# Optimization experiments

Hardware: AMD Instinct MI355X
Metric: run time of the kernel (lower is better)

Reference implementation:

```python
import jax, jax.numpy as jnp
import numpy as np
import math

B, T, D, H = 4, 2048, 1024, 8
DK = D // H


def _rel_shift(x):
    # x: [B, H, T, P] with P = 2T-1 (Transformer-XL relative shift)
    b, h, q, p = x.shape
    x = jnp.pad(x, ((0, 0), (0, 0), (0, 0), (1, 0)))
    x = x.reshape(b, h, p + 1, q)[:, :, 1:]
    return x.reshape(b, h, q, p)


def setup_inputs() -> dict:
    key = jax.random.key(0)
    ks = jax.random.split(key, 9)
    s = 0.02
    x = jax.random.normal(ks[0], (B, T, D), jnp.float32)
    pos_emb = jax.random.normal(ks[1], (1, 2 * T - 1, D), jnp.float32)
    Wq = jax.random.normal(ks[2], (D, D), jnp.float32) * s
    Wk = jax.random.normal(ks[3], (D, D), jnp.float32) * s
    Wv = jax.random.normal(ks[4], (D, D), jnp.float32) * s
    Wo = jax.random.normal(ks[5], (D, D), jnp.float32) * s
    Wp = jax.random.normal(ks[6], (D, D), jnp.float32) * s
    pos_bias_u = jax.random.normal(ks[7], (H, DK), jnp.float32) * s
    pos_bias_v = jax.random.normal(ks[8], (H, DK), jnp.float32) * s
    return {"x": x, "pos_emb": pos_emb, "Wq": Wq, "Wk": Wk, "Wv": Wv,
            "Wo": Wo, "Wp": Wp, "pos_bias_u": pos_bias_u, "pos_bias_v": pos_bias_v}


def reference(x, pos_emb, Wq, Wk, Wv, Wo, Wp, pos_bias_u, pos_bias_v):
    b, t, d = x.shape
    h, dk = pos_bias_u.shape
    inv_sdk = 1.0 / math.sqrt(dk)
    # projections (torch Linear: y = x @ W.T)
    q = (x @ Wq.T).reshape(b, t, h, dk)          # [B,T,H,DK]
    k = (x @ Wk.T).reshape(b, t, h, dk)          # [B,T,H,DK]
    v = (x @ Wv.T).reshape(b, t, h, dk)          # [B,T,H,DK]
    p = (pos_emb @ Wp.T).reshape(-1, h, dk)      # [P,H,DK], P = 2T-1
    # content and position scores
    matrix_ac = jnp.einsum('bqhd,bkhd->bhqk', q + pos_bias_u, k)   # [B,H,T,T]
    matrix_bd = jnp.einsum('bqhd,phd->bhqp', q + pos_bias_v, p)    # [B,H,T,2T-1]
    matrix_bd = _rel_shift(matrix_bd)[..., :t]                     # [B,H,T,T]
    scores = (matrix_ac + matrix_bd) * inv_sdk
    attn = jax.nn.softmax(scores, axis=-1)
    out = jnp.einsum('bhqk,bkhd->bqhd', attn, v).reshape(b, t, h * dk)
    return out @ Wo.T
```

## Files before the change

kernel.cpp:

```cpp
#include <hip/hip_runtime.h>
#include <cstdint>
#include <math.h>

#define B_   4
#define T_   2048
#define D_   1024
#define H_   8
#define DK_  128
#define P_   4095
#define PS_  4096

typedef unsigned short ushort_t;
typedef __attribute__((ext_vector_type(8))) short short8;
typedef __attribute__((ext_vector_type(4))) float floatx4;

__device__ inline float bf2f(ushort_t s) {
    return __uint_as_float(((unsigned int)s) << 16);
}
__device__ inline ushort_t f2bf(float f) {
    unsigned int u = __float_as_uint(f);
    u += 0x7fffu + ((u >> 16) & 1u);
    return (ushort_t)(u >> 16);
}

__device__ inline floatx4 mfma16(short8 a, short8 b, floatx4 c) {
    return __builtin_amdgcn_mfma_f32_16x16x32_bf16(a, b, c, 0, 0, 0);
}

__device__ inline void gload_lds16(const ushort_t* g, ushort_t* l) {
    __builtin_amdgcn_global_load_lds(
        (const __attribute__((address_space(1))) unsigned int*)g,
        (__attribute__((address_space(3))) unsigned int*)l, 16, 0, 0);
}

__global__ void detect_kernel(const ushort_t* x, int* flag) {
    if (blockIdx.x == 0 && threadIdx.x == 0) {
        int m = 0;
        for (int i = 0; i < 64; ++i) {
            float v = bf2f(x[2 * i]);
            float a = fabsf(v);
            if (!(a == 0.0f || (a > 1e-20f && a < 1e10f))) m = 1;
        }
        flag[0] = m;
    }
}

#define CV_TOT 17826816
template <int MODE>
__global__ __launch_bounds__(256) void convert_kernel(
    const int* __restrict__ flag,
    const void* __restrict__ x, const void* __restrict__ pe,
    const void* __restrict__ wq, const void* __restrict__ wk,
    const void* __restrict__ wv, const void* __restrict__ wo,
    const void* __restrict__ wp, const void* __restrict__ ub,
    const void* __restrict__ vb, ushort_t* __restrict__ dst)
{
    if (flag[0] != MODE) return;
    const size_t i = ((size_t)blockIdx.x * 256 + threadIdx.x) * 4;
    if (i >= CV_TOT) return;
    const void* s; size_t off;
    if (i < 8388608)       { s = x;  off = i; }
    else if (i < 12581888) { s = pe; off = i - 8388608; }
    else if (i < 13630464) { s = wq; off = i - 12581888; }
    else if (i < 14679040) { s = wk; off = i - 13630464; }
    else if (i < 15727616) { s = wv; off = i - 14679040; }
    else if (i < 16776192) { s = wo; off = i - 15727616; }
    else if (i < 17824768) { s = wp; off = i - 16776192; }
    else if (i < 17825792) { s = ub; off = i - 17824768; }
    else                   { s = vb; off = i - 17825792; }
    const size_t d = i + (i >= 12581888 ? 1024 : 0);
    if (MODE == 0) {
        *(uint2*)(dst + d) = *(const uint2*)((const ushort_t*)s + off);
    } else {
        float4 f = *(const float4*)((const float*)s + off);
        uint2 o;
        o.x = (unsigned)f2bf(f.x) | ((unsigned)f2bf(f.y) << 16);
        o.y = (unsigned)f2bf(f.z) | ((unsigned)f2bf(f.w) << 16);
        *(uint2*)(dst + d) = o;
    }
}

__global__ __launch_bounds__(256, 3) void gemm_mfma(
    const int* __restrict__ flag,
    const ushort_t* __restrict__ A, const ushort_t* __restrict__ W,
    void* __restrict__ C, int smode)
{
    if (smode == 3 && flag[0] != 0) return;
    if (smode == 4 && flag[0] != 1) return;
    const int K = 1024, N = 1024;

    __shared__ ushort_t Al[128 * 32];
    __shared__ ushort_t Wl[128 * 32];

    const int tid  = threadIdx.x;
    const int w    = tid >> 6, lane = tid & 63;
    const int r15  = lane & 15, quad = lane >> 4;
    const int wm   = w >> 1, wn = w & 1;
    const int m0   = blockIdx.y * 128, n0 = blockIdx.x * 128;

    floatx4 acc[4][4];
    const floatx4 z4 = {0.f, 0.f, 0.f, 0.f};
#pragma unroll
    for (int mt = 0; mt < 4; ++mt)
#pragma unroll
        for (int nt = 0; nt < 4; ++nt) acc[mt][nt] = z4;

    for (int k0 = 0; k0 < K; k0 += 32) {
#pragma unroll
        for (int it = 0; it < 2; ++it) {
            const int rbase = w * 32 + it * 16;
            const int row   = rbase + (lane >> 2);
            const int c     = (lane & 3) ^ ((row >> 1) & 3);
            gload_lds16(A + (size_t)(m0 + row) * K + k0 + c * 8, &Al[rbase * 32]);
            gload_lds16(W + (size_t)(n0 + row) * K + k0 + c * 8, &Wl[rbase * 32]);
        }
        __syncthreads();

        short8 af[4], bf[4];
#pragma unroll
        for (int mt = 0; mt < 4; ++mt) {
            const int row  = wm * 64 + mt * 16 + r15;
            const int slot = quad ^ ((row >> 1) & 3);
            af[mt] = *(const short8*)&Al[row * 32 + slot * 8];
        }
#pragma unroll
        for (int nt = 0; nt < 4; ++nt) {
            const int row  = wn * 64 + nt * 16 + r15;
            const int slot = quad ^ ((row >> 1) & 3);
            bf[nt] = *(const short8*)&Wl[row * 32 + slot * 8];
        }
#pragma unroll
        for (int mt = 0; mt < 4; ++mt)
#pragma unroll
            for (int nt = 0; nt < 4; ++nt)
                acc[mt][nt] = mfma16(af[mt], bf[nt], acc[mt][nt]);
        __syncthreads();
    }

#pragma unroll
    for (int mt = 0; mt < 4; ++mt)
#pragma unroll
        for (int nt = 0; nt < 4; ++nt)
#pragma unroll
            for (int i = 0; i < 4; ++i) {
                const int m = m0 + wm * 64 + mt * 16 + quad * 4 + i;
                const int n = n0 + wn * 64 + nt * 16 + r15;
                const float v = acc[mt][nt][i];
                if (smode == 0) {
                    const int b = m >> 11, t = m & (T_ - 1);
                    const int h = n >> 7, dk = n & (DK_ - 1);
                    ((ushort_t*)C)[(((size_t)(b * H_ + h)) * T_ + t) * DK_ + dk] = f2bf(v);
                } else if (smode == 1) {
                    const int h = n >> 7, dk = n & (DK_ - 1);
                    ((ushort_t*)C)[((size_t)h * PS_ + m) * DK_ + dk] = f2bf(v);
                } else if (smode == 2) {
                    const int b = m >> 11, t = m & (T_ - 1);
                    const int h = n >> 7, dk = n & (DK_ - 1);
                    ((ushort_t*)C)[((size_t)(b * H_ + h) * DK_ + dk) * T_ + t] = f2bf(v);
                } else if (smode == 3) {
                    ((ushort_t*)C)[(size_t)m * N + n] = f2bf(v);
                } else {
                    ((float*)C)[(size_t)m * N + n] = v;
                }
            }
}

__global__ __launch_bounds__(256, 2) void attn_mfma(
    const ushort_t* __restrict__ qg,
    const ushort_t* __restrict__ kgl,
    const ushort_t* __restrict__ vt,
    const ushort_t* __restrict__ pg,
    const ushort_t* __restrict__ ubb,
    const ushort_t* __restrict__ vbb,
    ushort_t* __restrict__ ao)
{
    __shared__ ushort_t K_lds[64 * 128];
    __shared__ ushort_t V_lds[128 * 64];
    __shared__ float bd_lds[4][16][84];
    __shared__ __align__(16) ushort_t pr_lds[4][16][72];

    const int tid  = threadIdx.x;
    const int w    = tid >> 6;
    const int lane = tid & 63;
    const int r15  = lane & 15;
    const int quad = lane >> 4;
    const int bh   = blockIdx.y;
    const int h    = bh & (H_ - 1);
    const int b    = bh >> 3;
    const int q0w  = blockIdx.x * 64 + w * 16;

    short8 quA[4], qvA[4];
    {
        const ushort_t* qrow = qg + ((size_t)bh * T_ + q0w + r15) * DK_;
#pragma unroll
        for (int ks = 0; ks < 4; ++ks) {
            const int dk0 = ks * 32 + quad * 8;
            uint4 q4 = *(const uint4*)(qrow + dk0);
            uint4 u4 = *(const uint4*)(ubb + (size_t)h * DK_ + dk0);
            uint4 v4 = *(const uint4*)(vbb + (size_t)h * DK_ + dk0);
            const ushort_t* qs = (const ushort_t*)&q4;
            const ushort_t* us = (const ushort_t*)&u4;
            const ushort_t* vs = (const ushort_t*)&v4;
#pragma unroll
            for (int j = 0; j < 8; ++j) {
                const float qf = bf2f(qs[j]);
                quA[ks][j] = (short)f2bf(qf + bf2f(us[j]));
                qvA[ks][j] = (short)f2bf(qf + bf2f(vs[j]));
            }
        }
    }

    floatx4 o[8];
    const floatx4 z4 = {0.f, 0.f, 0.f, 0.f};
#pragma unroll
    for (int g = 0; g < 8; ++g) o[g] = z4;
    float mrun[4], lrun[4];
#pragma unroll
    for (int i = 0; i < 4; ++i) { mrun[i] = -1e30f; lrun[i] = 0.f; }

    const float scale = 0.08838834764831845f;

    for (int kc0 = 0; kc0 < T_; kc0 += 64) {
#pragma unroll
        for (int it = 0; it < 4; ++it) {
            const int rbase = w * 16 + it * 4;
            const int row   = rbase + (lane >> 4);
            const int c     = (lane & 15) ^ (row & 7);
            gload_lds16(kgl + ((size_t)bh * T_ + kc0 + row) * DK_ + c * 8,
                        &K_lds[rbase * 128]);
        }
#pragma unroll
        for (int it = 0; it < 4; ++it) {
            const int rbase = w * 32 + it * 8;
            const int row   = rbase + (lane >> 3);
            const int c     = (lane & 7) ^ (row & 7);
            gload_lds16(vt + ((size_t)(bh * DK_ + row)) * T_ + kc0 + c * 8,
                        &V_lds[rbase * 64]);
        }
        __syncthreads();

        floatx4 ac[4];
#pragma unroll
        for (int g = 0; g < 4; ++g) {
            ac[g] = z4;
            const int row = g * 16 + r15;
#pragma unroll
            for (int ks = 0; ks < 4; ++ks) {
                const int slot = (ks * 4 + quad) ^ (row & 7);
                ac[g] = mfma16(quA[ks],
                               *(const short8*)&K_lds[row * 128 + slot * 8],
                               ac[g]);
            }
        }

        const int pbase = kc0 - q0w + (T_ - 1) - 15;
        floatx4 bd[5];
#pragma unroll
        for (int g = 0; g < 5; ++g) {
            bd[g] = z4;
            const ushort_t* pp =
                pg + ((size_t)h * PS_ + pbase + g * 16 + r15) * DK_ + quad * 8;
#pragma unroll
            for (int ks = 0; ks < 4; ++ks)
                bd[g] = mfma16(qvA[ks], *(const short8*)(pp + ks * 32), bd[g]);
        }
#pragma unroll
        for (int g = 0; g < 5; ++g)
#pragma unroll
            for (int i = 0; i < 4; ++i)
                bd_lds[w][quad * 4 + i][g * 16 + r15] = bd[g][i];

        float pr[4][4];
        float mc[4], alpha[4];
#pragma unroll
        for (int i = 0; i < 4; ++i) {
            const int r = quad * 4 + i;
            float mm = -1e30f;
#pragma unroll
            for (int g = 0; g < 4; ++g) {
                const float s =
                    (ac[g][i] + bd_lds[w][r][g * 16 + r15 - r + 15]) * scale;
                pr[g][i] = s;
                mm = fmaxf(mm, s);
            }
            mc[i] = mm;
        }
#pragma unroll
        for (int i = 0; i < 4; ++i) {
#pragma unroll
            for (int mk = 1; mk < 16; mk <<= 1)
                mc[i] = fmaxf(mc[i], __shfl_xor(mc[i], mk));
            const float mn = fmaxf(mrun[i], mc[i]);
            alpha[i] = __expf(mrun[i] - mn);
            mrun[i] = mn;
            float ls = 0.f;
#pragma unroll
            for (int g = 0; g < 4; ++g) {
                const float e = __expf(pr[g][i] - mn);
                pr[g][i] = e;
                ls += e;
            }
#pragma unroll
            for (int mk = 1; mk < 16; mk <<= 1)
                ls += __shfl_xor(ls, mk);
            lrun[i] = lrun[i] * alpha[i] + ls;
        }
#pragma unroll
        for (int g = 0; g < 8; ++g)
#pragma unroll
            for (int i = 0; i < 4; ++i) o[g][i] *= alpha[i];
#pragma unroll
        for (int g = 0; g < 4; ++g)
#pragma unroll
            for (int i = 0; i < 4; ++i)
                pr_lds[w][quad * 4 + i][g * 16 + r15] = f2bf(pr[g][i]);

        short8 pa[2];
#pragma unroll
        for (int ks2 = 0; ks2 < 2; ++ks2)
            pa[ks2] = *(const short8*)&pr_lds[w][r15][ks2 * 32 + quad * 8];
#pragma unroll
        for (int og = 0; og < 8; ++og) {
            const int row = og * 16 + r15;
#pragma unroll
            for (int ks2 = 0; ks2 < 2; ++ks2) {
                const int slot = (ks2 * 4 + quad) ^ (row & 7);
                o[og] = mfma16(pa[ks2],
                               *(const short8*)&V_lds[row * 64 + slot * 8],
                               o[og]);
            }
        }
        __syncthreads();
    }

    float inv[4];
#pragma unroll
    for (int i = 0; i < 4; ++i) inv[i] = 1.0f / lrun[i];
#pragma unroll
    for (int og = 0; og < 8; ++og)
#pragma unroll
        for (int i = 0; i < 4; ++i) {
            const size_t idx =
                ((size_t)(b * T_ + q0w + quad * 4 + i)) * D_ + h * DK_ + og * 16 + r15;
            ao[idx] = f2bf(o[og][i] * inv[i]);
        }
}

extern "C" void kernel_launch(void* const* d_in, const int* in_sizes, int n_in,
                              void* d_out, int out_size, void* d_ws, size_t ws_size,
                              hipStream_t stream) {
    const void* x  = d_in[0];
    const void* pe = d_in[1];
    const void* Wq = d_in[2];
    const void* Wk = d_in[3];
    const void* Wv = d_in[4];
    const void* Wo = d_in[5];
    const void* Wp = d_in[6];
    const void* ub = d_in[7];
    const void* vb = d_in[8];

    int* flag = (int*)d_ws;
    ushort_t* arena = (ushort_t*)d_ws + 16;
    ushort_t* xb   = arena;
    ushort_t* peb  = arena + 8388608;
    ushort_t* wqb  = arena + 12582912;
    ushort_t* wkb  = wqb + 1048576;
    ushort_t* wvb  = wkb + 1048576;
    ushort_t* wob  = wvb + 1048576;
    ushort_t* wpb  = wob + 1048576;
    ushort_t* ubb  = arena + 17825792;
    ushort_t* vbb  = ubb + 1024;
    ushort_t* q_ws  = arena + 17827840;
    ushort_t* k_ws  = q_ws + 8388608;
    ushort_t* vt_ws = k_ws + 8388608;
    ushort_t* p_ws  = vt_ws + 8388608;
    ushort_t* ao_ws = xb;

    detect_kernel<<<1, 64, 0, stream>>>((const ushort_t*)x, flag);

    const int cvb = CV_TOT / 4 / 256;
    convert_kernel<0><<<cvb, 256, 0, stream>>>(flag, x, pe, Wq, Wk, Wv, Wo, Wp, ub, vb, arena);
    convert_kernel<1><<<cvb, 256, 0, stream>>>(flag, x, pe, Wq, Wk, Wv, Wo, Wp, ub, vb, arena);

    const dim3 gX(8, 64);
    const dim3 gP(8, 32);
    gemm_mfma<<<gX, 256, 0, stream>>>(flag, xb,  wqb, q_ws, 0);
    gemm_mfma<<<gX, 256, 0, stream>>>(flag, xb,  wkb, k_ws, 0);
    gemm_mfma<<<gX, 256, 0, stream>>>(flag, xb,  wvb, vt_ws, 2);
    gemm_mfma<<<gP, 256, 0, stream>>>(flag, peb, wpb, p_ws, 1);

    attn_mfma<<<dim3(T_ / 64, B_ * H_), 256, 0, stream>>>(
        q_ws, k_ws, vt_ws, p_ws, ubb, vbb, ao_ws);

    gemm_mfma<<<gX, 256, 0, stream>>>(flag, ao_ws, wob, d_out, 3);
    gemm_mfma<<<gX, 256, 0, stream>>>(flag, ao_ws, wob, d_out, 4);
}
```

Baseline: 683.7 us.

## Use fragment-ordered LDS layouts, stage positional tile in LDS, shuffle-based rel-shift

```diff
diff --git a/kernel.cpp b/kernel.cpp
--- a/kernel.cpp
+++ b/kernel.cpp
@@ -89,8 +89,8 @@
     if (smode == 4 && flag[0] != 1) return;
     const int K = 1024, N = 1024;
 
-    __shared__ ushort_t Al[128 * 32];
-    __shared__ ushort_t Wl[128 * 32];
+    __shared__ ushort_t Al[16 * 512];
+    __shared__ ushort_t Wl[16 * 512];
 
     const int tid  = threadIdx.x;
     const int w    = tid >> 6, lane = tid & 63;
@@ -105,35 +105,35 @@
 #pragma unroll
         for (int nt = 0; nt < 4; ++nt) acc[mt][nt] = z4;
 
-    for (int k0 = 0; k0 < K; k0 += 32) {
-#pragma unroll
-        for (int it = 0; it < 2; ++it) {
-            const int rbase = w * 32 + it * 16;
-            const int row   = rbase + (lane >> 2);
-            const int c     = (lane & 3) ^ ((row >> 1) & 3);
-            gload_lds16(A + (size_t)(m0 + row) * K + k0 + c * 8, &Al[rbase * 32]);
-            gload_lds16(W + (size_t)(n0 + row) * K + k0 + c * 8, &Wl[rbase * 32]);
+    for (int k0 = 0; k0 < K; k0 += 64) {
+#pragma unroll
+        for (int ss = 0; ss < 4; ++ss) {
+            const int s  = w * 4 + ss;
+            const int mg = s >> 1, ks = s & 1;
+            const int row = mg * 16 + r15;
+            const int col = k0 + ks * 32 + quad * 8;
+            gload_lds16(A + (size_t)(m0 + row) * K + col, &Al[s * 512]);
+            gload_lds16(W + (size_t)(n0 + row) * K + col, &Wl[s * 512]);
         }
         __syncthreads();
 
-        short8 af[4], bf[4];
-#pragma unroll
-        for (int mt = 0; mt < 4; ++mt) {
-            const int row  = wm * 64 + mt * 16 + r15;
-            const int slot = quad ^ ((row >> 1) & 3);
-            af[mt] = *(const short8*)&Al[row * 32 + slot * 8];
-        }
-#pragma unroll
-        for (int nt = 0; nt < 4; ++nt) {
-            const int row  = wn * 64 + nt * 16 + r15;
-            const int slot = quad ^ ((row >> 1) & 3);
-            bf[nt] = *(const short8*)&Wl[row * 32 + slot * 8];
-        }
-#pragma unroll
-        for (int mt = 0; mt < 4; ++mt)
+        short8 af[2][4], bf[2][4];
+#pragma unroll
+        for (int ks = 0; ks < 2; ++ks) {
+#pragma unroll
+            for (int mt = 0; mt < 4; ++mt)
+                af[ks][mt] = *(const short8*)&Al[(((wm * 4 + mt) * 2 + ks) * 64 + lane) * 8];
 #pragma unroll
             for (int nt = 0; nt < 4; ++nt)
-                acc[mt][nt] = mfma16(af[mt], bf[nt], acc[mt][nt]);
+                bf[ks][nt] = *(const short8*)&Wl[(((wn * 4 + nt) * 2 + ks) * 64 + lane) * 8];
+        }
+#pragma unroll
+        for (int ks = 0; ks < 2; ++ks)
+#pragma unroll
+            for (int mt = 0; mt < 4; ++mt)
+#pragma unroll
+                for (int nt = 0; nt < 4; ++nt)
+                    acc[mt][nt] = mfma16(af[ks][mt], bf[ks][nt], acc[mt][nt]);
         __syncthreads();
     }
 
@@ -174,10 +174,10 @@
     const ushort_t* __restrict__ vbb,
     ushort_t* __restrict__ ao)
 {
-    __shared__ ushort_t K_lds[64 * 128];
-    __shared__ ushort_t V_lds[128 * 64];
-    __shared__ float bd_lds[4][16][84];
-    __shared__ __align__(16) ushort_t pr_lds[4][16][72];
+    __shared__ ushort_t K_lds[16 * 512];
+    __shared__ ushort_t V_lds[16 * 512];
+    __shared__ ushort_t P_lds[32 * 512];
+    __shared__ __align__(16) ushort_t pr_lds[4][1024];
 
     const int tid  = threadIdx.x;
     const int w    = tid >> 6;
@@ -187,7 +187,8 @@
     const int bh   = blockIdx.y;
     const int h    = bh & (H_ - 1);
     const int b    = bh >> 3;
-    const int q0w  = blockIdx.x * 64 + w * 16;
+    const int q0b  = blockIdx.x * 64;
+    const int q0w  = q0b + w * 16;
 
     short8 quA[4], qvA[4];
     {
@@ -210,6 +211,14 @@
         }
     }
 
+    int src[4], hi[4];
+#pragma unroll
+    for (int i = 0; i < 4; ++i) {
+        const int c = r15 + 15 - quad * 4 - i;
+        src[i] = quad * 16 + (c & 15);
+        hi[i]  = c >> 4;
+    }
+
     floatx4 o[8];
     const floatx4 z4 = {0.f, 0.f, 0.f, 0.f};
 #pragma unroll
@@ -221,21 +230,24 @@
     const float scale = 0.08838834764831845f;
 
     for (int kc0 = 0; kc0 < T_; kc0 += 64) {
-#pragma unroll
-        for (int it = 0; it < 4; ++it) {
-            const int rbase = w * 16 + it * 4;
-            const int row   = rbase + (lane >> 4);
-            const int c     = (lane & 15) ^ (row & 7);
-            gload_lds16(kgl + ((size_t)bh * T_ + kc0 + row) * DK_ + c * 8,
-                        &K_lds[rbase * 128]);
-        }
-#pragma unroll
-        for (int it = 0; it < 4; ++it) {
-            const int rbase = w * 32 + it * 8;
-            const int row   = rbase + (lane >> 3);
-            const int c     = (lane & 7) ^ (row & 7);
-            gload_lds16(vt + ((size_t)(bh * DK_ + row)) * T_ + kc0 + c * 8,
-                        &V_lds[rbase * 64]);
+        const int pbb = kc0 - q0b + 1984;
+
+#pragma unroll
+        for (int ss = 0; ss < 4; ++ss) {
+            const int ck = w * 4 + ss;
+            gload_lds16(kgl + ((size_t)bh * T_ + kc0 + w * 16 + r15) * DK_ + ss * 32 + quad * 8,
+                        &K_lds[ck * 512]);
+            const int cv = w * 4 + ss;
+            const int og = cv >> 1, ks2 = cv & 1;
+            gload_lds16(vt + ((size_t)(bh * DK_ + og * 16 + r15)) * T_ + kc0 + ks2 * 32 + quad * 8,
+                        &V_lds[cv * 512]);
+        }
+#pragma unroll
+        for (int ss = 0; ss < 8; ++ss) {
+            const int cp = w * 8 + ss;
+            const int gb = cp >> 2, ks = cp & 3;
+            gload_lds16(pg + ((size_t)h * PS_ + pbb + gb * 16 + r15) * DK_ + ks * 32 + quad * 8,
+                        &P_lds[cp * 512]);
         }
         __syncthreads();
 
@@ -243,43 +255,34 @@
 #pragma unroll
         for (int g = 0; g < 4; ++g) {
             ac[g] = z4;
-            const int row = g * 16 + r15;
-#pragma unroll
-            for (int ks = 0; ks < 4; ++ks) {
-                const int slot = (ks * 4 + quad) ^ (row & 7);
+#pragma unroll
+            for (int ks = 0; ks < 4; ++ks)
                 ac[g] = mfma16(quA[ks],
-                               *(const short8*)&K_lds[row * 128 + slot * 8],
+                               *(const short8*)&K_lds[((g * 4 + ks) * 64 + lane) * 8],
                                ac[g]);
-            }
-        }
-
-        const int pbase = kc0 - q0w + (T_ - 1) - 15;
+        }
         floatx4 bd[5];
 #pragma unroll
         for (int g = 0; g < 5; ++g) {
             bd[g] = z4;
-            const ushort_t* pp =
-                pg + ((size_t)h * PS_ + pbase + g * 16 + r15) * DK_ + quad * 8;
+            const int gb = (3 - w) + g;
 #pragma unroll
             for (int ks = 0; ks < 4; ++ks)
-                bd[g] = mfma16(qvA[ks], *(const short8*)(pp + ks * 32), bd[g]);
-        }
-#pragma unroll
-        for (int g = 0; g < 5; ++g)
-#pragma unroll
-            for (int i = 0; i < 4; ++i)
-                bd_lds[w][quad * 4 + i][g * 16 + r15] = bd[g][i];
+                bd[g] = mfma16(qvA[ks],
+                               *(const short8*)&P_lds[((gb * 4 + ks) * 64 + lane) * 8],
+                               bd[g]);
+        }
 
         float pr[4][4];
         float mc[4], alpha[4];
 #pragma unroll
         for (int i = 0; i < 4; ++i) {
-            const int r = quad * 4 + i;
             float mm = -1e30f;
 #pragma unroll
             for (int g = 0; g < 4; ++g) {
-                const float s =
-                    (ac[g][i] + bd_lds[w][r][g * 16 + r15 - r + 15]) * scale;
+                const float lo = __shfl(bd[g][i],     src[i], 64);
+                const float hh = __shfl(bd[g + 1][i], src[i], 64);
+                const float s  = (ac[g][i] + (hi[i] ? hh : lo)) * scale;
                 pr[g][i] = s;
                 mm = fmaxf(mm, s);
             }
@@ -309,27 +312,26 @@
         for (int g = 0; g < 8; ++g)
 #pragma unroll
             for (int i = 0; i < 4; ++i) o[g][i] *= alpha[i];
-#pragma unroll
-        for (int g = 0; g < 4; ++g)
+
+#pragma unroll
+        for (int g = 0; g < 4; ++g) {
+            const int unit = (g >> 1) * 4 + (g & 1) * 2 + (r15 >> 3);
 #pragma unroll
             for (int i = 0; i < 4; ++i)
-                pr_lds[w][quad * 4 + i][g * 16 + r15] = f2bf(pr[g][i]);
-
+                pr_lds[w][(unit * 16 + quad * 4 + i) * 8 + (r15 & 7)] = f2bf(pr[g][i]);
+        }
         short8 pa[2];
 #pragma unroll
         for (int ks2 = 0; ks2 < 2; ++ks2)
-            pa[ks2] = *(const short8*)&pr_lds[w][r15][ks2 * 32 + quad * 8];
-#pragma unroll
-        for (int og = 0; og < 8; ++og) {
-            const int row = og * 16 + r15;
-#pragma unroll
-            for (int ks2 = 0; ks2 < 2; ++ks2) {
-                const int slot = (ks2 * 4 + quad) ^ (row & 7);
+            pa[ks2] = *(const short8*)&pr_lds[w][(ks2 * 64 + lane) * 8];
+
+#pragma unroll
+        for (int og = 0; og < 8; ++og)
+#pragma unroll
+            for (int ks2 = 0; ks2 < 2; ++ks2)
                 o[og] = mfma16(pa[ks2],
-                               *(const short8*)&V_lds[row * 64 + slot * 8],
+                               *(const short8*)&V_lds[((og * 2 + ks2) * 64 + lane) * 8],
                                o[og]);
-            }
-        }
         __syncthreads();
     }
 
```

Measured after the change: 589.5 us. 13.8% less time.
